# Kernel tuning notes

Hardware: AMD Instinct MI355X
Metric: run time of the kernel (lower is better)

Reference implementation:

```python
import jax, jax.numpy as jnp
import numpy as np

# TT-factorized linear: 784 = 7*4*7*4 -> 512 = 4*4*8*4, max_rank=20
# canonical TT ranks: [1, 20, 20, 16, 1] (r3 capped by m4*n4 = 16)
B = 16384
R1, R2, R3 = 20, 20, 16


def setup_inputs() -> dict:
    key = jax.random.key(0)
    k = jax.random.split(key, 6)
    x = jax.random.normal(k[0], (B, 784), jnp.float32)
    # TT cores G_k[r_{k-1}, m_k, n_k, r_k] with boundary ranks squeezed
    core1 = jax.random.normal(k[1], (7, 4, R1), jnp.float32) * 0.3   # [m1,n1,r1]
    core2 = jax.random.normal(k[2], (R1, 4, 4, R2), jnp.float32) * 0.1  # [r1,m2,n2,r2]
    core3 = jax.random.normal(k[3], (R2, 7, 8, R3), jnp.float32) * 0.05  # [r2,m3,n3,r3]
    core4 = jax.random.normal(k[4], (R3, 4, 4), jnp.float32) * 0.1   # [r3,m4,n4]
    bias = jax.random.normal(k[5], (512,), jnp.float32) * 0.01
    return {"x": x, "core1": core1, "core2": core2, "core3": core3,
            "core4": core4, "bias": bias}


def reference(x, core1, core2, core3, core4, bias):
    b = x.shape[0]
    # reshape input into TT mode factorization [B, m1, m2, m3, m4]
    x5 = x.reshape(b, 7, 4, 7, 4)
    # chain of small core contractions (the fusion-opportunity op pattern)
    t = jnp.einsum('bijkl,ipr->bjklpr', x5, core1)   # [B,4,7,4, n1,r1]
    t = jnp.einsum('bjklpr,rjqs->bklpqs', t, core2)  # [B,7,4, n1,n2,r2]
    t = jnp.einsum('bklpqs,sket->blpqet', t, core3)  # [B,4, n1,n2,n3,r3]
    y = jnp.einsum('blpqet,tlf->bpqef', t, core4)    # [B, n1,n2,n3,n4]
    y = y.reshape(b, 512) + bias
    # original forward: relu then softmax over features.
    # NOTE: the source calls self.fc2(y) but discards the result, so it is
    # omitted here (no effect on output).
    return jax.nn.softmax(jax.nn.relu(y), axis=1)
```

## Files before the change

### kernel.cpp

```cpp
#include <hip/hip_runtime.h>


typedef __attribute__((ext_vector_type(8))) short short8;
typedef __attribute__((ext_vector_type(4))) float floatx4;

__device__ __forceinline__ unsigned int pack2_bf16(float a, float b) {
    unsigned int ua = __float_as_uint(a);
    unsigned int ub = __float_as_uint(b);
    return ((ub + 0x8000u) & 0xFFFF0000u) | ((ua + 0x8000u) >> 16);
}

__device__ __forceinline__ short f32_to_bf16_rne(float v) {
    unsigned int u = __float_as_uint(v);
    return (short)(((u + 0x7FFFu + ((u >> 16) & 1)) >> 16) & 0xFFFF);
}

__global__ void prep_all(const float* __restrict__ c1, const float* __restrict__ c2,
                         const float* __restrict__ c3, const float* __restrict__ c4,
                         short* __restrict__ wp) {
    const int tid = threadIdx.x;
    const int blk = blockIdx.x;
    if (blk == 224) {
        for (int e = tid; e < 8192; e += 256) {
            int j   = e & 7;
            int lid = (e >> 3) & 15;
            int q2  = (e >> 7) & 1;
            int tn  = e >> 8;
            wp[(((tn * 25 + 24) * 64 + (2 + q2) * 16 + lid) << 3) + j] = 0;
        }
        return;
    }
    __shared__ float t12s[320];
    __shared__ float t123s[7 * 256];
    __shared__ float c4s[256];

    const int ij    = blk >> 3;
    const int strip = blk & 7;
    const int i  = ij >> 2, j2 = ij & 3;
    const int p  = strip >> 1;
    const int qh = strip & 1;

    if (tid < 256) c4s[tid] = c4[tid];
    for (int e = tid; e < 320; e += 256) {
        int s = e % 20, pq = e / 20;
        int pp = pq >> 2, q = pq & 3;
        float acc = 0.f;
        #pragma unroll
        for (int r = 0; r < 20; ++r)
            acc += c1[i * 80 + pp * 20 + r] * c2[r * 320 + j2 * 80 + q * 20 + s];
        t12s[e] = acc;
    }
    __syncthreads();

    for (int e = tid; e < 1792; e += 256) {
        int k3 = e >> 8, li = e & 255;
        int t = li & 15, pql = li >> 4;
        int qloc = pql >> 3, e3 = pql & 7;
        int q = 2 * qh + qloc;
        float acc = 0.f;
        const float* tp = t12s + (p * 4 + q) * 20;
        const float* cp = c3 + k3 * 128 + e3 * 16 + t;
        #pragma unroll
        for (int s = 0; s < 20; ++s) acc += tp[s] * cp[s * 896];
        t123s[e] = acc;
    }
    __syncthreads();

    for (int e = tid; e < 1792; e += 256) {
        int kl = e >> 6, nl = e & 63;
        int k = ij * 28 + kl;
        int n = strip * 64 + nl;
        int k3 = kl >> 2, l = kl & 3;
        int f4 = n & 3, e3 = (n >> 2) & 7;
        int pql = ((n >> 5) & 1) * 8 + e3;
        const float* tp = t123s + k3 * 256 + pql * 16;
        const float* cq = c4s + l * 4 + f4;
        float a = 0.f;
        #pragma unroll
        for (int t = 0; t < 16; ++t) a += tp[t] * cq[t * 16];
        int tk = k >> 5, quad = (k >> 3) & 3, j = k & 7;
        int tn = n >> 4, lid = n & 15;
        wp[(((tn * 25 + tk) * 64 + quad * 16 + lid) << 3) + j] = f32_to_bf16_rne(a);
    }
}

__global__ __launch_bounds__(512, 4) void tt_gemm(const float* __restrict__ x,
                                                  const short* __restrict__ wp,
                                                  const float* __restrict__ bias,
                                                  float* __restrict__ out) {
    __shared__ __align__(16) short s_a[3200 * 8];
    __shared__ float part[8][32];

    const int tid  = threadIdx.x;
    const int w    = tid >> 6;
    const int lane = tid & 63;
    const int quad = lane >> 4;
    const int lid  = lane & 15;
    const int m_base = blockIdx.x * 32;

    const short* wpw = wp + ((size_t)(w * 4) * 25 * 64 + lane) * 8;

    short8 b_f[3][4];
    #pragma unroll
    for (int nt = 0; nt < 4; ++nt) {
        b_f[0][nt] = *(const short8*)(wpw + (size_t)(nt * 25 + 0) * 64 * 8);
        b_f[1][nt] = *(const short8*)(wpw + (size_t)(nt * 25 + 1) * 64 * 8);
    }

    for (int a = tid; a < 3200; a += 512) {
        const int row = ((a >> 6) & 1) * 16 + (a & 15);
        const int kc  = ((a >> 7) * 4 + ((a >> 4) & 3)) * 8;
        floatx4 v0 = {0.f, 0.f, 0.f, 0.f}, v1 = {0.f, 0.f, 0.f, 0.f};
        if (kc < 784) {
            const floatx4* pp = (const floatx4*)(x + (size_t)(m_base + row) * 784 + kc);
            v0 = pp[0]; v1 = pp[1];
        }
        union { short8 s; unsigned int u[4]; } af;
        af.u[0] = pack2_bf16(v0.x, v0.y);
        af.u[1] = pack2_bf16(v0.z, v0.w);
        af.u[2] = pack2_bf16(v1.x, v1.y);
        af.u[3] = pack2_bf16(v1.z, v1.w);
        *(short8*)&s_a[a * 8] = af.s;
    }
    __syncthreads();

    const short* sa = s_a + lane * 8;

    floatx4 acc[2][4];
    #pragma unroll
    for (int mt = 0; mt < 2; ++mt)
        #pragma unroll
        for (int nt = 0; nt < 4; ++nt)
            acc[mt][nt] = floatx4{0.f, 0.f, 0.f, 0.f};

    short8 a_f[2][2];
    a_f[0][0] = *(const short8*)(sa);
    a_f[0][1] = *(const short8*)(sa + 64 * 8);

    #pragma unroll
    for (int tk = 0; tk < 25; ++tk) {
        if (tk + 2 < 25) {
            #pragma unroll
            for (int nt = 0; nt < 4; ++nt)
                b_f[(tk + 2) % 3][nt] = *(const short8*)(wpw + (size_t)(nt * 25 + tk + 2) * 64 * 8);
        }
        if (tk + 1 < 25) {
            const short* sa2 = sa + (size_t)(tk + 1) * 128 * 8;
            a_f[(tk + 1) & 1][0] = *(const short8*)(sa2);
            a_f[(tk + 1) & 1][1] = *(const short8*)(sa2 + 64 * 8);
        }
        #pragma unroll
        for (int nt = 0; nt < 4; ++nt) {
            acc[0][nt] = __builtin_amdgcn_mfma_f32_16x16x32_bf16(a_f[tk & 1][0], b_f[tk % 3][nt], acc[0][nt], 0, 0, 0);
            acc[1][nt] = __builtin_amdgcn_mfma_f32_16x16x32_bf16(a_f[tk & 1][1], b_f[tk % 3][nt], acc[1][nt], 0, 0, 0);
        }
    }

    float bias_v[4];
    #pragma unroll
    for (int nt = 0; nt < 4; ++nt)
        bias_v[nt] = bias[w * 64 + nt * 16 + lid];

    #pragma unroll
    for (int mt = 0; mt < 2; ++mt) {
        #pragma unroll
        for (int reg = 0; reg < 4; ++reg) {
            float s = 0.f;
            #pragma unroll
            for (int nt = 0; nt < 4; ++nt) {
                float v = acc[mt][nt][reg] + bias_v[nt];
                v = fmaxf(v, 0.f);
                float e = __expf(v);
                acc[mt][nt][reg] = e;
                s += e;
            }
            s += __shfl_xor(s, 1, 64);
            s += __shfl_xor(s, 2, 64);
            s += __shfl_xor(s, 4, 64);
            s += __shfl_xor(s, 8, 64);
            if (lid == 0) part[w][mt * 16 + quad * 4 + reg] = s;
        }
    }
    __syncthreads();

    #pragma unroll
    for (int mt = 0; mt < 2; ++mt) {
        #pragma unroll
        for (int reg = 0; reg < 4; ++reg) {
            const int row = mt * 16 + quad * 4 + reg;
            float tot = 0.f;
            #pragma unroll
            for (int ww = 0; ww < 8; ++ww) tot += part[ww][row];
            const float inv = 1.0f / tot;
            #pragma unroll
            for (int nt = 0; nt < 4; ++nt)
                out[(size_t)(m_base + row) * 512 + w * 64 + nt * 16 + lid] = acc[mt][nt][reg] * inv;
        }
    }
}

extern "C" void kernel_launch(void* const* d_in, const int* in_sizes, int n_in,
                              void* d_out, int out_size, void* d_ws, size_t ws_size,
                              hipStream_t stream) {
    const float* x    = (const float*)d_in[0];
    const float* c1   = (const float*)d_in[1];
    const float* c2   = (const float*)d_in[2];
    const float* c3   = (const float*)d_in[3];
    const float* c4   = (const float*)d_in[4];
    const float* bias = (const float*)d_in[5];
    float* out = (float*)d_out;
    short* wpb = (short*)d_ws;

    prep_all<<<225, 256, 0, stream>>>(c1, c2, c3, c4, wpb);
    tt_gemm <<<512, 512, 0, stream>>>(x, wpb, bias, out);
}
```

Baseline: 126.2 us.

## Double M tile to 64 rows and overlap tail A-tile loads with MFMA

Each block now handles 64 rows instead of 32, so every B fragment loaded from global memory feeds twice as many MFMAs, and the grid shrinks to 256 blocks. The A staging is split: K-chunks 0-17 are converted and stored up front, while the global loads for chunks 18-24 are issued into registers before the first MFMA phase and written to shared memory after it. This hides part of the x load latency behind compute. The cost is more registers and LDS per block (occupancy bound lowered to 2), and only 256 blocks, which may underfill the GPU.

```diff
diff --git a/kernel.cpp b/kernel.cpp
--- a/kernel.cpp
+++ b/kernel.cpp
@@ -84,19 +84,19 @@
     }
 }
 
-__global__ __launch_bounds__(512, 4) void tt_gemm(const float* __restrict__ x,
+__global__ __launch_bounds__(512, 2) void tt_gemm(const float* __restrict__ x,
                                                   const short* __restrict__ wp,
                                                   const float* __restrict__ bias,
                                                   float* __restrict__ out) {
-    __shared__ __align__(16) short s_a[3200 * 8];
-    __shared__ float part[8][32];
+    __shared__ __align__(16) short s_a[6400 * 8];
+    __shared__ float part[8][64];
 
     const int tid  = threadIdx.x;
     const int w    = tid >> 6;
     const int lane = tid & 63;
     const int quad = lane >> 4;
     const int lid  = lane & 15;
-    const int m_base = blockIdx.x * 32;
+    const int m_base = blockIdx.x * 64;
 
     const short* wpw = wp + ((size_t)(w * 4) * 25 * 64 + lane) * 8;
 
@@ -107,14 +107,29 @@
         b_f[1][nt] = *(const short8*)(wpw + (size_t)(nt * 25 + 1) * 64 * 8);
     }
 
-    for (int a = tid; a < 3200; a += 512) {
-        const int row = ((a >> 6) & 1) * 16 + (a & 15);
-        const int kc  = ((a >> 7) * 4 + ((a >> 4) & 3)) * 8;
-        floatx4 v0 = {0.f, 0.f, 0.f, 0.f}, v1 = {0.f, 0.f, 0.f, 0.f};
-        if (kc < 784) {
-            const floatx4* pp = (const floatx4*)(x + (size_t)(m_base + row) * 784 + kc);
-            v0 = pp[0]; v1 = pp[1];
-        }
+    floatx4 h0[4], h1[4];
+    #pragma unroll
+    for (int i = 0; i < 4; ++i) {
+        h0[i] = floatx4{0.f, 0.f, 0.f, 0.f};
+        h1[i] = floatx4{0.f, 0.f, 0.f, 0.f};
+        const int c = 4608 + tid + i * 512;
+        if (c < 6400) {
+            const int row = ((c >> 6) & 3) * 16 + (c & 15);
+            const int kc  = ((c >> 8) * 4 + ((c >> 4) & 3)) * 8;
+            if (kc < 784) {
+                const floatx4* pp = (const floatx4*)(x + (size_t)(m_base + row) * 784 + kc);
+                h0[i] = pp[0]; h1[i] = pp[1];
+            }
+        }
+    }
+
+    #pragma unroll
+    for (int it = 0; it < 9; ++it) {
+        const int a   = tid + it * 512;
+        const int row = ((a >> 6) & 3) * 16 + (a & 15);
+        const int kc  = ((a >> 8) * 4 + ((a >> 4) & 3)) * 8;
+        const floatx4* pp = (const floatx4*)(x + (size_t)(m_base + row) * 784 + kc);
+        floatx4 v0 = pp[0], v1 = pp[1];
         union { short8 s; unsigned int u[4]; } af;
         af.u[0] = pack2_bf16(v0.x, v0.y);
         af.u[1] = pack2_bf16(v0.z, v0.w);
@@ -126,34 +141,72 @@
 
     const short* sa = s_a + lane * 8;
 
-    floatx4 acc[2][4];
-    #pragma unroll
-    for (int mt = 0; mt < 2; ++mt)
+    floatx4 acc[4][4];
+    #pragma unroll
+    for (int mt = 0; mt < 4; ++mt)
         #pragma unroll
         for (int nt = 0; nt < 4; ++nt)
             acc[mt][nt] = floatx4{0.f, 0.f, 0.f, 0.f};
 
-    short8 a_f[2][2];
-    a_f[0][0] = *(const short8*)(sa);
-    a_f[0][1] = *(const short8*)(sa + 64 * 8);
-
-    #pragma unroll
-    for (int tk = 0; tk < 25; ++tk) {
+    short8 a_f[2][4];
+    #pragma unroll
+    for (int mt = 0; mt < 4; ++mt)
+        a_f[0][mt] = *(const short8*)(sa + (size_t)(mt * 64) * 8);
+
+    #pragma unroll
+    for (int tk = 0; tk < 18; ++tk) {
+        #pragma unroll
+        for (int nt = 0; nt < 4; ++nt)
+            b_f[(tk + 2) % 3][nt] = *(const short8*)(wpw + (size_t)(nt * 25 + tk + 2) * 64 * 8);
+        if (tk + 1 < 18) {
+            const short* sa2 = sa + (size_t)(tk + 1) * 256 * 8;
+            #pragma unroll
+            for (int mt = 0; mt < 4; ++mt)
+                a_f[(tk + 1) & 1][mt] = *(const short8*)(sa2 + (size_t)(mt * 64) * 8);
+        }
+        #pragma unroll
+        for (int nt = 0; nt < 4; ++nt)
+            #pragma unroll
+            for (int mt = 0; mt < 4; ++mt)
+                acc[mt][nt] = __builtin_amdgcn_mfma_f32_16x16x32_bf16(a_f[tk & 1][mt], b_f[tk % 3][nt], acc[mt][nt], 0, 0, 0);
+    }
+
+    #pragma unroll
+    for (int i = 0; i < 4; ++i) {
+        const int c = 4608 + tid + i * 512;
+        if (c < 6400) {
+            union { short8 s; unsigned int u[4]; } af;
+            af.u[0] = pack2_bf16(h0[i].x, h0[i].y);
+            af.u[1] = pack2_bf16(h0[i].z, h0[i].w);
+            af.u[2] = pack2_bf16(h1[i].x, h1[i].y);
+            af.u[3] = pack2_bf16(h1[i].z, h1[i].w);
+            *(short8*)&s_a[c * 8] = af.s;
+        }
+    }
+    __syncthreads();
+
+    #pragma unroll
+    for (int mt = 0; mt < 4; ++mt)
+        a_f[0][mt] = *(const short8*)(sa + ((size_t)18 * 256 + mt * 64) * 8);
+
+    #pragma unroll
+    for (int tk = 18; tk < 25; ++tk) {
         if (tk + 2 < 25) {
             #pragma unroll
             for (int nt = 0; nt < 4; ++nt)
                 b_f[(tk + 2) % 3][nt] = *(const short8*)(wpw + (size_t)(nt * 25 + tk + 2) * 64 * 8);
         }
         if (tk + 1 < 25) {
-            const short* sa2 = sa + (size_t)(tk + 1) * 128 * 8;
-            a_f[(tk + 1) & 1][0] = *(const short8*)(sa2);
-            a_f[(tk + 1) & 1][1] = *(const short8*)(sa2 + 64 * 8);
-        }
-        #pragma unroll
-        for (int nt = 0; nt < 4; ++nt) {
-            acc[0][nt] = __builtin_amdgcn_mfma_f32_16x16x32_bf16(a_f[tk & 1][0], b_f[tk % 3][nt], acc[0][nt], 0, 0, 0);
-            acc[1][nt] = __builtin_amdgcn_mfma_f32_16x16x32_bf16(a_f[tk & 1][1], b_f[tk % 3][nt], acc[1][nt], 0, 0, 0);
-        }
+            const short* sa2 = sa + (size_t)(tk + 1) * 256 * 8;
+            #pragma unroll
+            for (int mt = 0; mt < 4; ++mt)
+                a_f[(tk + 1) & 1][mt] = *(const short8*)(sa2 + (size_t)(mt * 64) * 8);
+        }
+        #pragma unroll
+        for (int nt = 0; nt < 4; ++nt)
+            #pragma unroll
+            for (int mt = 0; mt < 4; ++mt)
+                acc[mt][nt] = __builtin_amdgcn_mfma_f32_16x16x32_bf16(a_f[tk & 1][mt], b_f[tk % 3][nt], acc[mt][nt], 0, 0, 0);
     }
 
     float bias_v[4];
@@ -162,7 +215,7 @@
         bias_v[nt] = bias[w * 64 + nt * 16 + lid];
 
     #pragma unroll
-    for (int mt = 0; mt < 2; ++mt) {
+    for (int mt = 0; mt < 4; ++mt) {
         #pragma unroll
         for (int reg = 0; reg < 4; ++reg) {
             float s = 0.f;
@@ -184,7 +237,7 @@
     __syncthreads();
 
     #pragma unroll
-    for (int mt = 0; mt < 2; ++mt) {
+    for (int mt = 0; mt < 4; ++mt) {
         #pragma unroll
         for (int reg = 0; reg < 4; ++reg) {
             const int row = mt * 16 + quad * 4 + reg;
@@ -212,5 +265,5 @@
     short* wpb = (short*)d_ws;
 
     prep_all<<<225, 256, 0, stream>>>(c1, c2, c3, c4, wpb);
-    tt_gemm <<<512, 512, 0, stream>>>(x, wpb, bias, out);
-}
+    tt_gemm <<<256, 512, 0, stream>>>(x, wpb, bias, out);
+}
```

Result: no change. 125.3 us (-0.8%).
